# Kernel optimization log

Hardware: AMD Instinct MI355X
Metric: run time of the kernel (lower is better)

Reference implementation:

```python
import jax, jax.numpy as jnp
import numpy as np

N_ATOM_TYPES = 100
N_BOND_TYPES = 10
N_NODES = 10000
N_EDGES = 320000
N_CAND = 100000
HID = 256
N_MP = 3


def setup_inputs() -> dict:
    key = jax.random.key(0)
    ks = jax.random.split(key, 16)
    d = HID
    inp = {
        "atom_types": jax.random.randint(ks[0], (N_NODES,), 0, N_ATOM_TYPES),
        "bond_types": jax.random.randint(ks[1], (N_EDGES,), 0, N_BOND_TYPES),
        "edge_index": jax.random.randint(ks[2], (2, N_EDGES), 0, N_NODES),
        "candidates": jax.random.randint(ks[3], (N_CAND, 2), 0, N_NODES),
        # parameters (weights stored as [in, out]; bias [out])
        "atom_embed": jax.random.normal(ks[4], (N_ATOM_TYPES, d)) * 0.02,
        "atom_W": jax.random.normal(ks[5], (d, d)) / np.sqrt(d),
        "atom_b": jnp.zeros((d,)),
        "bond_embed": jax.random.normal(ks[6], (N_BOND_TYPES, d)) * 0.02,
        "bond_W": jax.random.normal(ks[7], (d, d)) / np.sqrt(d),
        "bond_b": jnp.zeros((d,)),
        "conv_W": jax.random.normal(ks[8], (N_MP, d, d)) / np.sqrt(d),
        "conv_b": jnp.zeros((N_MP, d)),
        "s_W1": jax.random.normal(ks[9], (2 * d, d)) / np.sqrt(2 * d),
        "s_b1": jnp.zeros((d,)),
        "s_W2": jax.random.normal(ks[10], (d, 1)) / np.sqrt(d),
        "s_b2": jnp.zeros((1,)),
    }
    return inp


def _wln_forward(atom_types, bond_types, edge_index, candidates,
                 atom_embed, atom_W, atom_b, bond_embed, bond_W, bond_b,
                 conv_W, conv_b, s_W1, s_b1, s_W2, s_b2):
    # encoders
    h = atom_embed[atom_types] @ atom_W + atom_b            # [N, d]
    e = bond_embed[bond_types] @ bond_W + bond_b            # [E, d] (unused downstream, as in the original forward)
    del e

    src, dst = edge_index[0], edge_index[1]
    n = h.shape[0]
    ones = jnp.ones((src.shape[0],), dtype=h.dtype)
    deg_out = jax.ops.segment_sum(ones, src, num_segments=n)
    deg_in = jax.ops.segment_sum(ones, dst, num_segments=n)
    norm_src = jnp.where(deg_out > 0, deg_out ** -0.5, 0.0)[:, None]  # [N,1]
    norm_dst = jnp.where(deg_in > 0, deg_in ** -0.5, 0.0)[:, None]

    # message passing: DGL GraphConv norm='both' + ReLU
    for i in range(conv_W.shape[0]):
        m = (h * norm_src)[src]                             # [E, d]
        agg = jax.ops.segment_sum(m, dst, num_segments=n)   # [N, d]
        h = jax.nn.relu((agg * norm_dst) @ conv_W[i] + conv_b[i])

    # batched candidate scorer: gather + concat + 2-layer MLP
    u, v = candidates[:, 0], candidates[:, 1]
    pair = jnp.concatenate([h[u], h[v]], axis=-1)           # [C, 2d]
    hid = jax.nn.relu(pair @ s_W1 + s_b1)                   # [C, d]
    scores = hid @ s_W2 + s_b2                              # [C, 1]
    return scores.squeeze(-1)                               # [C]


def reference(atom_types, bond_types, edge_index, candidates,
              atom_embed, atom_W, atom_b, bond_embed, bond_W, bond_b,
              conv_W, conv_b, s_W1, s_b1, s_W2, s_b2):
    return _wln_forward(atom_types, bond_types, edge_index, candidates,
                        atom_embed, atom_W, atom_b, bond_embed, bond_W, bond_b,
                        conv_W, conv_b, s_W1, s_b1, s_W2, s_b2)
```

## Files before the change

### kernel.cpp

```cpp
#include <hip/hip_runtime.h>

#define N_NODES 10000
#define N_EDGES 320000
#define N_CAND  100000
#define HID     256
#define N_MP    3
#define N_ATYPE 100

static __device__ __forceinline__ float relu_f(float x) { return x > 0.f ? x : 0.f; }

static __device__ __forceinline__ void gemm_core(
    const float* __restrict__ A, const float* __restrict__ B,
    const float* __restrict__ bias, float* __restrict__ C,
    int M, int mb, int nb, int doRelu)
{
    __shared__ float As[32][68];
    __shared__ float Bs[32][68];

    int tid = threadIdx.x;
    int tx = tid & 15;
    int ty = tid >> 4;

    float acc[8][4] = {};

    for (int k0 = 0; k0 < 256; k0 += 32) {
        #pragma unroll
        for (int p = 0; p < 4; ++p) {
            int flat = p * 128 + tid;
            int row  = flat >> 3;
            int kc   = flat & 7;
            float4 av = make_float4(0.f, 0.f, 0.f, 0.f);
            if (mb + row < M)
                av = *(const float4*)(A + (size_t)(mb + row) * 256 + k0 + kc * 4);
            As[kc * 4 + 0][row] = av.x;
            As[kc * 4 + 1][row] = av.y;
            As[kc * 4 + 2][row] = av.z;
            As[kc * 4 + 3][row] = av.w;
        }
        #pragma unroll
        for (int p = 0; p < 4; ++p) {
            int flat = p * 128 + tid;
            int row  = flat >> 4;
            int c    = flat & 15;
            *(float4*)(&Bs[row][c * 4]) =
                *(const float4*)(B + (size_t)(k0 + row) * 256 + nb + c * 4);
        }
        __syncthreads();

        #pragma unroll
        for (int k = 0; k < 32; ++k) {
            float4 a0 = *(const float4*)(&As[k][ty * 8]);
            float4 a1 = *(const float4*)(&As[k][ty * 8 + 4]);
            float4 b4 = *(const float4*)(&Bs[k][tx * 4]);
            float a[8] = {a0.x, a0.y, a0.z, a0.w, a1.x, a1.y, a1.z, a1.w};
            float b[4] = {b4.x, b4.y, b4.z, b4.w};
            #pragma unroll
            for (int i = 0; i < 8; ++i)
                #pragma unroll
                for (int j = 0; j < 4; ++j)
                    acc[i][j] = fmaf(a[i], b[j], acc[i][j]);
        }
        __syncthreads();
    }

    float bvv[4] = {0.f, 0.f, 0.f, 0.f};
    if (bias) {
        float4 bv = *(const float4*)(bias + nb + tx * 4);
        bvv[0] = bv.x; bvv[1] = bv.y; bvv[2] = bv.z; bvv[3] = bv.w;
    }
    #pragma unroll
    for (int i = 0; i < 8; ++i) {
        int row = mb + ty * 8 + i;
        if (row >= M) continue;
        float r[4];
        #pragma unroll
        for (int j = 0; j < 4; ++j) {
            r[j] = acc[i][j] + bvv[j];
            if (doRelu) r[j] = relu_f(r[j]);
        }
        *(float4*)(C + (size_t)row * 256 + nb + tx * 4) =
            make_float4(r[0], r[1], r[2], r[3]);
    }
}

__global__ __launch_bounds__(128) void k_gemm(
    const float* __restrict__ A, const float* __restrict__ B,
    const float* __restrict__ bias, float* __restrict__ C,
    int M, int doRelu)
{
    gemm_core(A, B, bias, C, M, blockIdx.x * 64, blockIdx.y * 64, doRelu);
}

__global__ __launch_bounds__(128) void k_gemm_pq(
    const float* __restrict__ A, const float* __restrict__ W1,
    float* __restrict__ P, float* __restrict__ Q, int M)
{
    int half = blockIdx.y >> 2;
    const float* B = W1 + (size_t)half * 256 * 256;
    float* C = half ? Q : P;
    gemm_core(A, B, nullptr, C, M, blockIdx.x * 64, (blockIdx.y & 3) * 64, 0);
}

__global__ void k_hist(const int* __restrict__ ei,
                       int* __restrict__ dout, int* __restrict__ din)
{
    int e = blockIdx.x * blockDim.x + threadIdx.x;
    if (e >= N_EDGES) return;
    atomicAdd(&dout[ei[e]], 1);
    atomicAdd(&din[ei[N_EDGES + e]], 1);
}

__global__ void k_norm(const int* __restrict__ dout, const int* __restrict__ din,
                       float* __restrict__ ns, float* __restrict__ nd)
{
    int i = blockIdx.x * blockDim.x + threadIdx.x;
    if (i >= N_NODES) return;
    int o = dout[i], in = din[i];
    ns[i] = (o  > 0) ? (1.0f / sqrtf((float)o))  : 0.f;
    nd[i] = (in > 0) ? (1.0f / sqrtf((float)in)) : 0.f;
}

__global__ __launch_bounds__(256) void k_h0(const int* __restrict__ types,
                                            const float* __restrict__ E0,
                                            float* __restrict__ h)
{
    int node = blockIdx.x * 4 + (threadIdx.x >> 6);
    int lane = threadIdx.x & 63;
    if (node >= N_NODES) return;
    int t = types[node];
    ((float4*)h)[node * 64 + lane] = ((const float4*)E0)[t * 64 + lane];
}

__global__ __launch_bounds__(256) void k_scan(const int* __restrict__ deg,
                                              int* __restrict__ off, int n)
{
    __shared__ int part[256];
    int t = threadIdx.x;
    int chunk = (n + 255) / 256;
    int base = t * chunk;
    int s = 0;
    for (int i = 0; i < chunk; ++i) {
        int idx = base + i;
        if (idx < n) s += deg[idx];
    }
    part[t] = s;
    __syncthreads();
    for (int d = 1; d < 256; d <<= 1) {
        int v = (t >= d) ? part[t - d] : 0;
        __syncthreads();
        part[t] += v;
        __syncthreads();
    }
    int run = (t == 0) ? 0 : part[t - 1];
    if (t == 0) off[0] = 0;
    for (int i = 0; i < chunk; ++i) {
        int idx = base + i;
        if (idx < n) { run += deg[idx]; off[idx + 1] = run; }
    }
}

__global__ void k_fill(const int* __restrict__ ei, const int* __restrict__ off,
                       int* __restrict__ cur, int* __restrict__ csr)
{
    int e = blockIdx.x * blockDim.x + threadIdx.x;
    if (e >= N_EDGES) return;
    int d = ei[N_EDGES + e];
    int p = off[d] + atomicAdd(&cur[d], 1);
    csr[p] = ei[e];
}

__global__ __launch_bounds__(256) void k_agg(
    const float* __restrict__ h, const float* __restrict__ ns,
    const float* __restrict__ nd, const int* __restrict__ off,
    const int* __restrict__ csr, float* __restrict__ out)
{
    int node = blockIdx.x * 4 + (threadIdx.x >> 6);
    int lane = threadIdx.x & 63;
    if (node >= N_NODES) return;
    int s0 = off[node], s1 = off[node + 1];
    const float4* h4 = (const float4*)h;

    float4 acc0 = make_float4(0.f, 0.f, 0.f, 0.f);
    float4 acc1 = make_float4(0.f, 0.f, 0.f, 0.f);

    int e = s0;
    for (; e + 4 <= s1; e += 4) {
        int i0 = csr[e], i1 = csr[e + 1], i2 = csr[e + 2], i3 = csr[e + 3];
        float w0 = ns[i0], w1 = ns[i1], w2 = ns[i2], w3 = ns[i3];
        float4 v0 = h4[(size_t)i0 * 64 + lane];
        float4 v1 = h4[(size_t)i1 * 64 + lane];
        float4 v2 = h4[(size_t)i2 * 64 + lane];
        float4 v3 = h4[(size_t)i3 * 64 + lane];
        acc0.x = fmaf(v0.x, w0, acc0.x); acc0.y = fmaf(v0.y, w0, acc0.y);
        acc0.z = fmaf(v0.z, w0, acc0.z); acc0.w = fmaf(v0.w, w0, acc0.w);
        acc1.x = fmaf(v1.x, w1, acc1.x); acc1.y = fmaf(v1.y, w1, acc1.y);
        acc1.z = fmaf(v1.z, w1, acc1.z); acc1.w = fmaf(v1.w, w1, acc1.w);
        acc0.x = fmaf(v2.x, w2, acc0.x); acc0.y = fmaf(v2.y, w2, acc0.y);
        acc0.z = fmaf(v2.z, w2, acc0.z); acc0.w = fmaf(v2.w, w2, acc0.w);
        acc1.x = fmaf(v3.x, w3, acc1.x); acc1.y = fmaf(v3.y, w3, acc1.y);
        acc1.z = fmaf(v3.z, w3, acc1.z); acc1.w = fmaf(v3.w, w3, acc1.w);
    }
    for (; e < s1; ++e) {
        int s = csr[e];
        float w = ns[s];
        float4 hv = h4[(size_t)s * 64 + lane];
        acc0.x = fmaf(hv.x, w, acc0.x); acc0.y = fmaf(hv.y, w, acc0.y);
        acc0.z = fmaf(hv.z, w, acc0.z); acc0.w = fmaf(hv.w, w, acc0.w);
    }
    float d = nd[node];
    float4 r;
    r.x = (acc0.x + acc1.x) * d;
    r.y = (acc0.y + acc1.y) * d;
    r.z = (acc0.z + acc1.z) * d;
    r.w = (acc0.w + acc1.w) * d;
    ((float4*)out)[node * 64 + lane] = r;
}

__global__ __launch_bounds__(256) void k_score(
    const int* __restrict__ cand, const float* __restrict__ P,
    const float* __restrict__ Q, const float* __restrict__ b1,
    const float* __restrict__ W2, const float* __restrict__ b2,
    float* __restrict__ out)
{
    int c = blockIdx.x * 4 + (threadIdx.x >> 6);
    int lane = threadIdx.x & 63;
    if (c >= N_CAND) return;
    int u = cand[2 * c];
    int v = cand[2 * c + 1];
    float4 p = ((const float4*)P)[(size_t)u * 64 + lane];
    float4 q = ((const float4*)Q)[(size_t)v * 64 + lane];
    float4 b = ((const float4*)b1)[lane];
    float4 w = ((const float4*)W2)[lane];
    float hx = relu_f(p.x + q.x + b.x);
    float hy = relu_f(p.y + q.y + b.y);
    float hz = relu_f(p.z + q.z + b.z);
    float hw = relu_f(p.w + q.w + b.w);
    float d = hx * w.x + hy * w.y + hz * w.z + hw * w.w;
    #pragma unroll
    for (int o = 32; o > 0; o >>= 1)
        d += __shfl_xor(d, o, 64);
    if (lane == 0) out[c] = d + b2[0];
}

extern "C" void kernel_launch(void* const* d_in, const int* in_sizes, int n_in,
                              void* d_out, int out_size, void* d_ws, size_t ws_size,
                              hipStream_t stream)
{
    const int*   atom_types = (const int*)d_in[0];
    const int*   edge_index = (const int*)d_in[2];
    const int*   candidates = (const int*)d_in[3];
    const float* atom_embed = (const float*)d_in[4];
    const float* atom_W     = (const float*)d_in[5];
    const float* atom_b     = (const float*)d_in[6];
    const float* conv_W     = (const float*)d_in[10];
    const float* conv_b     = (const float*)d_in[11];
    const float* s_W1       = (const float*)d_in[12];
    const float* s_b1       = (const float*)d_in[13];
    const float* s_W2       = (const float*)d_in[14];
    const float* s_b2       = (const float*)d_in[15];
    float* out = (float*)d_out;

    char* w = (char*)d_ws;
    size_t o = 0;
    auto alloc = [&](size_t bytes) {
        void* p = w + o;
        o += (bytes + 255) & ~(size_t)255;
        return p;
    };
    float* h0  = (float*)alloc((size_t)N_NODES * HID * 4);
    float* h1  = (float*)alloc((size_t)N_NODES * HID * 4);
    float* agg = (float*)alloc((size_t)N_NODES * HID * 4);
    float* E0  = (float*)alloc((size_t)N_ATYPE * HID * 4);
    int*   ints = (int*)alloc((size_t)3 * N_NODES * 4);
    float* ns  = (float*)alloc((size_t)N_NODES * 4);
    float* nd  = (float*)alloc((size_t)N_NODES * 4);
    int*   off = (int*)alloc((size_t)(N_NODES + 1) * 4);
    int*   csr = (int*)alloc((size_t)N_EDGES * 4);
    int* dego = ints;
    int* degi = ints + N_NODES;
    int* cur  = ints + 2 * N_NODES;

    hipMemsetAsync(ints, 0, (size_t)3 * N_NODES * 4, stream);

    k_gemm<<<dim3(2, 4), 128, 0, stream>>>(atom_embed, atom_W, atom_b, E0, N_ATYPE, 0);

    k_hist<<<(N_EDGES + 255) / 256, 256, 0, stream>>>(edge_index, dego, degi);
    k_norm<<<(N_NODES + 255) / 256, 256, 0, stream>>>(dego, degi, ns, nd);
    k_h0<<<N_NODES / 4, 256, 0, stream>>>(atom_types, E0, h0);
    k_scan<<<1, 256, 0, stream>>>(degi, off, N_NODES);
    k_fill<<<(N_EDGES + 255) / 256, 256, 0, stream>>>(edge_index, off, cur, csr);

    const float* hc = h0;
    float* hn = h1;
    const int GX = (N_NODES + 63) / 64;
    for (int i = 0; i < N_MP; ++i) {
        k_agg<<<N_NODES / 4, 256, 0, stream>>>(hc, ns, nd, off, csr, agg);
        k_gemm<<<dim3(GX, 4), 128, 0, stream>>>(
            agg, conv_W + (size_t)i * HID * HID, conv_b + (size_t)i * HID, hn, N_NODES, 1);
        float* t = (float*)hc; hc = hn; hn = t;
    }
    float* P = agg;
    float* Q = hn;
    k_gemm_pq<<<dim3(GX, 8), 128, 0, stream>>>(hc, s_W1, P, Q, N_NODES);

    k_score<<<N_CAND / 4, 256, 0, stream>>>(candidates, P, Q, s_b1, s_W2, s_b2, out);
}
```

Before: 418.2 us.

## Split aggregation and scoring by column slices, prescale by source norm, swizzle GEMM grids

The aggregation and scoring kernels now split the 256 feature columns into slices handled by separate blocks, with blocks for one column slice laid out adjacently. This narrows the working set of gathered rows per slice to improve cache reuse. The source-degree norm is folded into the producing kernels (h0 and the conv GEMM epilogue), which removes the per-edge ns loads and multiplies. The GEMM grids are remapped to 1D with an 8-wide swizzle, scoring writes per-slice partial sums that a second kernel reduces, and the scan uses 1024 threads. The cost is an extra kernel launch and an 8xN_CAND partial buffer, plus narrower scalar loads in place of float4 loads.

```diff
diff --git a/kernel.cpp b/kernel.cpp
--- a/kernel.cpp
+++ b/kernel.cpp
@@ -11,8 +11,8 @@
 
 static __device__ __forceinline__ void gemm_core(
     const float* __restrict__ A, const float* __restrict__ B,
-    const float* __restrict__ bias, float* __restrict__ C,
-    int M, int mb, int nb, int doRelu)
+    const float* __restrict__ bias, const float* __restrict__ scale,
+    float* __restrict__ C, int M, int mb, int nb, int doRelu)
 {
     __shared__ float As[32][68];
     __shared__ float Bs[32][68];
@@ -72,11 +72,13 @@
     for (int i = 0; i < 8; ++i) {
         int row = mb + ty * 8 + i;
         if (row >= M) continue;
+        float sc = scale ? scale[row] : 1.0f;
         float r[4];
         #pragma unroll
         for (int j = 0; j < 4; ++j) {
             r[j] = acc[i][j] + bvv[j];
             if (doRelu) r[j] = relu_f(r[j]);
+            r[j] *= sc;
         }
         *(float4*)(C + (size_t)row * 256 + nb + tx * 4) =
             make_float4(r[0], r[1], r[2], r[3]);
@@ -88,17 +90,39 @@
     const float* __restrict__ bias, float* __restrict__ C,
     int M, int doRelu)
 {
-    gemm_core(A, B, bias, C, M, blockIdx.x * 64, blockIdx.y * 64, doRelu);
+    gemm_core(A, B, bias, nullptr, C, M, blockIdx.x * 64, blockIdx.y * 64, doRelu);
+}
+
+__global__ __launch_bounds__(128) void k_gemm_conv(
+    const float* __restrict__ A, const float* __restrict__ B,
+    const float* __restrict__ bias, const float* __restrict__ scale,
+    float* __restrict__ C, int M)
+{
+    int bid = blockIdx.x;
+    int l = bid & 7;
+    int r = bid >> 3;
+    int y = r & 3;
+    int g = r >> 2;
+    int x = g * 8 + l;
+    if (x * 64 >= M) return;
+    gemm_core(A, B, bias, scale, C, M, x * 64, y * 64, 1);
 }
 
 __global__ __launch_bounds__(128) void k_gemm_pq(
     const float* __restrict__ A, const float* __restrict__ W1,
     float* __restrict__ P, float* __restrict__ Q, int M)
 {
-    int half = blockIdx.y >> 2;
+    int bid = blockIdx.x;
+    int l = bid & 7;
+    int r = bid >> 3;
+    int y = r & 7;
+    int g = r >> 3;
+    int x = g * 8 + l;
+    if (x * 64 >= M) return;
+    int half = y >> 2;
     const float* B = W1 + (size_t)half * 256 * 256;
     float* C = half ? Q : P;
-    gemm_core(A, B, nullptr, C, M, blockIdx.x * 64, (blockIdx.y & 3) * 64, 0);
+    gemm_core(A, B, nullptr, nullptr, C, M, x * 64, (y & 3) * 64, 0);
 }
 
 __global__ void k_hist(const int* __restrict__ ei,
@@ -122,21 +146,25 @@
 
 __global__ __launch_bounds__(256) void k_h0(const int* __restrict__ types,
                                             const float* __restrict__ E0,
+                                            const float* __restrict__ ns,
                                             float* __restrict__ h)
 {
     int node = blockIdx.x * 4 + (threadIdx.x >> 6);
     int lane = threadIdx.x & 63;
     if (node >= N_NODES) return;
     int t = types[node];
-    ((float4*)h)[node * 64 + lane] = ((const float4*)E0)[t * 64 + lane];
-}
-
-__global__ __launch_bounds__(256) void k_scan(const int* __restrict__ deg,
-                                              int* __restrict__ off, int n)
-{
-    __shared__ int part[256];
+    float s = ns[node];
+    float4 v = ((const float4*)E0)[t * 64 + lane];
+    v.x *= s; v.y *= s; v.z *= s; v.w *= s;
+    ((float4*)h)[node * 64 + lane] = v;
+}
+
+__global__ __launch_bounds__(1024) void k_scan(const int* __restrict__ deg,
+                                               int* __restrict__ off, int n)
+{
+    __shared__ int part[1024];
     int t = threadIdx.x;
-    int chunk = (n + 255) / 256;
+    int chunk = (n + 1023) / 1024;
     int base = t * chunk;
     int s = 0;
     for (int i = 0; i < chunk; ++i) {
@@ -145,7 +173,7 @@
     }
     part[t] = s;
     __syncthreads();
-    for (int d = 1; d < 256; d <<= 1) {
+    for (int d = 1; d < 1024; d <<= 1) {
         int v = (t >= d) ? part[t - d] : 0;
         __syncthreads();
         part[t] += v;
@@ -170,76 +198,69 @@
 }
 
 __global__ __launch_bounds__(256) void k_agg(
-    const float* __restrict__ h, const float* __restrict__ ns,
-    const float* __restrict__ nd, const int* __restrict__ off,
-    const int* __restrict__ csr, float* __restrict__ out)
-{
-    int node = blockIdx.x * 4 + (threadIdx.x >> 6);
+    const float* __restrict__ h, const float* __restrict__ nd,
+    const int* __restrict__ off, const int* __restrict__ csr,
+    float* __restrict__ out)
+{
+    int bid  = blockIdx.x;
+    int slot = bid & 7;
+    int c    = slot >> 1;
+    int grp  = ((bid >> 3) << 1) | (slot & 1);
+    int wave = threadIdx.x >> 6;
     int lane = threadIdx.x & 63;
-    if (node >= N_NODES) return;
+    int node = grp * 4 + wave;
+    int col  = c * 64 + lane;
+
     int s0 = off[node], s1 = off[node + 1];
-    const float4* h4 = (const float4*)h;
-
-    float4 acc0 = make_float4(0.f, 0.f, 0.f, 0.f);
-    float4 acc1 = make_float4(0.f, 0.f, 0.f, 0.f);
-
+    float acc0 = 0.f, acc1 = 0.f, acc2 = 0.f, acc3 = 0.f;
     int e = s0;
     for (; e + 4 <= s1; e += 4) {
         int i0 = csr[e], i1 = csr[e + 1], i2 = csr[e + 2], i3 = csr[e + 3];
-        float w0 = ns[i0], w1 = ns[i1], w2 = ns[i2], w3 = ns[i3];
-        float4 v0 = h4[(size_t)i0 * 64 + lane];
-        float4 v1 = h4[(size_t)i1 * 64 + lane];
-        float4 v2 = h4[(size_t)i2 * 64 + lane];
-        float4 v3 = h4[(size_t)i3 * 64 + lane];
-        acc0.x = fmaf(v0.x, w0, acc0.x); acc0.y = fmaf(v0.y, w0, acc0.y);
-        acc0.z = fmaf(v0.z, w0, acc0.z); acc0.w = fmaf(v0.w, w0, acc0.w);
-        acc1.x = fmaf(v1.x, w1, acc1.x); acc1.y = fmaf(v1.y, w1, acc1.y);
-        acc1.z = fmaf(v1.z, w1, acc1.z); acc1.w = fmaf(v1.w, w1, acc1.w);
-        acc0.x = fmaf(v2.x, w2, acc0.x); acc0.y = fmaf(v2.y, w2, acc0.y);
-        acc0.z = fmaf(v2.z, w2, acc0.z); acc0.w = fmaf(v2.w, w2, acc0.w);
-        acc1.x = fmaf(v3.x, w3, acc1.x); acc1.y = fmaf(v3.y, w3, acc1.y);
-        acc1.z = fmaf(v3.z, w3, acc1.z); acc1.w = fmaf(v3.w, w3, acc1.w);
-    }
-    for (; e < s1; ++e) {
-        int s = csr[e];
-        float w = ns[s];
-        float4 hv = h4[(size_t)s * 64 + lane];
-        acc0.x = fmaf(hv.x, w, acc0.x); acc0.y = fmaf(hv.y, w, acc0.y);
-        acc0.z = fmaf(hv.z, w, acc0.z); acc0.w = fmaf(hv.w, w, acc0.w);
-    }
-    float d = nd[node];
-    float4 r;
-    r.x = (acc0.x + acc1.x) * d;
-    r.y = (acc0.y + acc1.y) * d;
-    r.z = (acc0.z + acc1.z) * d;
-    r.w = (acc0.w + acc1.w) * d;
-    ((float4*)out)[node * 64 + lane] = r;
-}
-
-__global__ __launch_bounds__(256) void k_score(
+        float v0 = h[(size_t)i0 * 256 + col];
+        float v1 = h[(size_t)i1 * 256 + col];
+        float v2 = h[(size_t)i2 * 256 + col];
+        float v3 = h[(size_t)i3 * 256 + col];
+        acc0 += v0; acc1 += v1; acc2 += v2; acc3 += v3;
+    }
+    for (; e < s1; ++e)
+        acc0 += h[(size_t)csr[e] * 256 + col];
+    out[(size_t)node * 256 + col] = (acc0 + acc1 + acc2 + acc3) * nd[node];
+}
+
+__global__ __launch_bounds__(256) void k_score_part(
     const int* __restrict__ cand, const float* __restrict__ P,
     const float* __restrict__ Q, const float* __restrict__ b1,
-    const float* __restrict__ W2, const float* __restrict__ b2,
-    float* __restrict__ out)
-{
-    int c = blockIdx.x * 4 + (threadIdx.x >> 6);
+    const float* __restrict__ W2, float* __restrict__ part)
+{
+    int bid  = blockIdx.x;
+    int c    = bid & 7;
+    int grp  = bid >> 3;
+    int wave = threadIdx.x >> 6;
     int lane = threadIdx.x & 63;
-    if (c >= N_CAND) return;
-    int u = cand[2 * c];
-    int v = cand[2 * c + 1];
-    float4 p = ((const float4*)P)[(size_t)u * 64 + lane];
-    float4 q = ((const float4*)Q)[(size_t)v * 64 + lane];
-    float4 b = ((const float4*)b1)[lane];
-    float4 w = ((const float4*)W2)[lane];
-    float hx = relu_f(p.x + q.x + b.x);
-    float hy = relu_f(p.y + q.y + b.y);
-    float hz = relu_f(p.z + q.z + b.z);
-    float hw = relu_f(p.w + q.w + b.w);
-    float d = hx * w.x + hy * w.y + hz * w.z + hw * w.w;
+    int half = lane >> 5;
+    int l    = lane & 31;
+    int cd   = grp * 8 + wave * 2 + half;
+    int col  = c * 32 + l;
+
+    int u = cand[2 * cd];
+    int v = cand[2 * cd + 1];
+    float x = P[(size_t)u * 256 + col] + Q[(size_t)v * 256 + col] + b1[col];
+    x = relu_f(x) * W2[col];
     #pragma unroll
-    for (int o = 32; o > 0; o >>= 1)
-        d += __shfl_xor(d, o, 64);
-    if (lane == 0) out[c] = d + b2[0];
+    for (int o = 16; o > 0; o >>= 1)
+        x += __shfl_xor(x, o, 64);
+    if (l == 0) part[(size_t)c * N_CAND + cd] = x;
+}
+
+__global__ void k_sred(const float* __restrict__ part,
+                       const float* __restrict__ b2, float* __restrict__ out)
+{
+    int i = blockIdx.x * 256 + threadIdx.x;
+    if (i >= N_CAND) return;
+    float s = b2[0];
+    #pragma unroll
+    for (int c = 0; c < 8; ++c) s += part[(size_t)c * N_CAND + i];
+    out[i] = s;
 }
 
 extern "C" void kernel_launch(void* const* d_in, const int* in_sizes, int n_in,
@@ -267,15 +288,16 @@
         o += (bytes + 255) & ~(size_t)255;
         return p;
     };
-    float* h0  = (float*)alloc((size_t)N_NODES * HID * 4);
-    float* h1  = (float*)alloc((size_t)N_NODES * HID * 4);
-    float* agg = (float*)alloc((size_t)N_NODES * HID * 4);
-    float* E0  = (float*)alloc((size_t)N_ATYPE * HID * 4);
+    float* h0   = (float*)alloc((size_t)N_NODES * HID * 4);
+    float* h1   = (float*)alloc((size_t)N_NODES * HID * 4);
+    float* agg  = (float*)alloc((size_t)N_NODES * HID * 4);
+    float* E0   = (float*)alloc((size_t)N_ATYPE * HID * 4);
+    float* part = (float*)alloc((size_t)8 * N_CAND * 4);
     int*   ints = (int*)alloc((size_t)3 * N_NODES * 4);
-    float* ns  = (float*)alloc((size_t)N_NODES * 4);
-    float* nd  = (float*)alloc((size_t)N_NODES * 4);
-    int*   off = (int*)alloc((size_t)(N_NODES + 1) * 4);
-    int*   csr = (int*)alloc((size_t)N_EDGES * 4);
+    float* ns   = (float*)alloc((size_t)N_NODES * 4);
+    float* nd   = (float*)alloc((size_t)N_NODES * 4);
+    int*   off  = (int*)alloc((size_t)(N_NODES + 1) * 4);
+    int*   csr  = (int*)alloc((size_t)N_EDGES * 4);
     int* dego = ints;
     int* degi = ints + N_NODES;
     int* cur  = ints + 2 * N_NODES;
@@ -286,22 +308,24 @@
 
     k_hist<<<(N_EDGES + 255) / 256, 256, 0, stream>>>(edge_index, dego, degi);
     k_norm<<<(N_NODES + 255) / 256, 256, 0, stream>>>(dego, degi, ns, nd);
-    k_h0<<<N_NODES / 4, 256, 0, stream>>>(atom_types, E0, h0);
-    k_scan<<<1, 256, 0, stream>>>(degi, off, N_NODES);
+    k_h0<<<N_NODES / 4, 256, 0, stream>>>(atom_types, E0, ns, h0);
+    k_scan<<<1, 1024, 0, stream>>>(degi, off, N_NODES);
     k_fill<<<(N_EDGES + 255) / 256, 256, 0, stream>>>(edge_index, off, cur, csr);
 
     const float* hc = h0;
     float* hn = h1;
-    const int GX = (N_NODES + 63) / 64;
     for (int i = 0; i < N_MP; ++i) {
-        k_agg<<<N_NODES / 4, 256, 0, stream>>>(hc, ns, nd, off, csr, agg);
-        k_gemm<<<dim3(GX, 4), 128, 0, stream>>>(
-            agg, conv_W + (size_t)i * HID * HID, conv_b + (size_t)i * HID, hn, N_NODES, 1);
+        k_agg<<<N_NODES, 256, 0, stream>>>(hc, nd, off, csr, agg);
+        const float* sc = (i < N_MP - 1) ? ns : nullptr;
+        k_gemm_conv<<<640, 128, 0, stream>>>(
+            agg, conv_W + (size_t)i * HID * HID, conv_b + (size_t)i * HID,
+            sc, hn, N_NODES);
         float* t = (float*)hc; hc = hn; hn = t;
     }
     float* P = agg;
     float* Q = hn;
-    k_gemm_pq<<<dim3(GX, 8), 128, 0, stream>>>(hc, s_W1, P, Q, N_NODES);
-
-    k_score<<<N_CAND / 4, 256, 0, stream>>>(candidates, P, Q, s_b1, s_W2, s_b2, out);
-}
+    k_gemm_pq<<<1280, 128, 0, stream>>>(hc, s_W1, P, Q, N_NODES);
+
+    k_score_part<<<N_CAND, 256, 0, stream>>>(candidates, P, Q, s_b1, s_W2, part);
+    k_sred<<<(N_CAND + 255) / 256, 256, 0, stream>>>(part, s_b2, out);
+}
```

Result: no change. 418.2 us (+0.0%).
